# Kernel tuning notes

Hardware: AMD Instinct MI355X
Metric: run time of the kernel (lower is better)

The kernel has to match this reference:

```python
import jax, jax.numpy as jnp
import numpy as np

N = 50000
E = 625000
IN_NODE = 128
IN_EDGE = 64
H = 128
OUT = 112
L = 3


def setup_inputs() -> dict:
    key = jax.random.key(0)
    ks = jax.random.split(key, 16)
    s = lambda fan_in: 1.0 / np.sqrt(fan_in)
    inp = {
        "x": jax.random.normal(ks[0], (N, IN_NODE), jnp.float32),
        "edge_attr": jax.random.normal(ks[1], (E, IN_EDGE), jnp.float32),
        "edge_index": jax.random.randint(ks[2], (2, E), 0, N, jnp.int32),
        # encoders
        "node_W": jax.random.uniform(ks[3], (IN_NODE, H), jnp.float32, -s(IN_NODE), s(IN_NODE)),
        "node_b": jnp.zeros((H,), jnp.float32),
        "edge_W": jax.random.uniform(ks[4], (IN_EDGE, H), jnp.float32, -s(IN_EDGE), s(IN_EDGE)),
        "edge_b": jnp.zeros((H,), jnp.float32),
        # per-layer GINConv MLP params, stacked over layers
        "W1": jax.random.uniform(ks[5], (L, H, 2 * H), jnp.float32, -s(H), s(H)),
        "b1": jnp.zeros((L, 2 * H), jnp.float32),
        "W2": jax.random.uniform(ks[6], (L, 2 * H, H), jnp.float32, -s(2 * H), s(2 * H)),
        "b2": jnp.zeros((L, H), jnp.float32),
        "eps": jnp.zeros((L,), jnp.float32),
        # output head
        "lin_W": jax.random.uniform(ks[7], (H, OUT), jnp.float32, -s(H), s(H)),
        "lin_b": jnp.zeros((OUT,), jnp.float32),
    }
    return inp


def reference(x, edge_attr, edge_index, node_W, node_b, edge_W, edge_b,
              W1, b1, W2, b2, eps, lin_W, lin_b):
    src = edge_index[0]  # x_j gather indices (source nodes)
    dst = edge_index[1]  # scatter targets
    n = x.shape[0]

    x = x @ node_W + node_b                 # [N, H]
    ea = edge_attr @ edge_W + edge_b        # [E, H]

    # in-degree for mean aggregation (clamped at 1, zero-degree -> 0 agg)
    deg = jax.ops.segment_sum(jnp.ones((src.shape[0],), x.dtype), dst, num_segments=n)
    inv_deg = 1.0 / jnp.maximum(deg, 1.0)   # [N]

    for l in range(L):
        msg = x[src] + ea                                    # [E, H]
        agg = jax.ops.segment_sum(msg, dst, num_segments=n)  # [N, H]
        agg = agg * inv_deg[:, None]                         # mean
        h = (1.0 + eps[l]) * x + agg
        h = jax.nn.relu(h @ W1[l] + b1[l]) @ W2[l] + b2[l]   # GIN MLP
        x = jax.nn.relu(h)                                   # dropout is identity in eval

    return x @ lin_W + lin_b                 # [N, OUT]
```

## Files before the change

### kernel.cpp

```cpp
#include <hip/hip_runtime.h>


typedef unsigned short u16;
typedef unsigned int   u32;

using short8 = __attribute__((ext_vector_type(8))) short;
using f32x4  = __attribute__((ext_vector_type(4))) float;

__device__ __forceinline__ float b2f(u16 u) {
  union { u32 i; float f; } v; v.i = ((u32)u) << 16; return v.f;
}
__device__ __forceinline__ u16 f2b(float f) {
  union { float f; u32 i; } v; v.f = f;
  u32 i = v.i;
  return (u16)((i + 0x7FFFu + ((i >> 16) & 1u)) >> 16);
}

__global__ void sniff_kernel(const u16* __restrict__ xu, int* __restrict__ flag) {
  __shared__ int cnt;
  if (threadIdx.x == 0) cnt = 0;
  __syncthreads();
  int c = 0;
  for (int i = threadIdx.x; i < 1024; i += 256) {
    int e = (xu[i] >> 7) & 0xFF;
    if (e >= 100 && e <= 140) c++;
  }
  atomicAdd(&cnt, c);
  __syncthreads();
  if (threadIdx.x == 0) *flag = (cnt >= 820) ? 1 : 0;
}

__global__ void cvt_bf16_kernel(const void* __restrict__ src, u16* __restrict__ dst,
                                int n, const int* __restrict__ flag) {
  int i = blockIdx.x * 256 + threadIdx.x;
  if (i >= n) return;
  if (*flag) dst[i] = ((const u16*)src)[i];
  else       dst[i] = f2b(((const float*)src)[i]);
}

__global__ void cvt_f32_kernel(const void* __restrict__ src, float* __restrict__ dst,
                               int n, const int* __restrict__ flag) {
  int i = blockIdx.x * 256 + threadIdx.x;
  if (i >= n) return;
  if (*flag) dst[i] = b2f(((const u16*)src)[i]);
  else       dst[i] = ((const float*)src)[i];
}

__global__ void deg_kernel(const int* __restrict__ dst, int* __restrict__ deg, int e) {
  int i = blockIdx.x * 256 + threadIdx.x;
  if (i < e) atomicAdd(&deg[dst[i]], 1);
}

__global__ void scanA_kernel(const int* __restrict__ deg, int* __restrict__ rowptr,
                             float* __restrict__ invdeg, int* __restrict__ btot, int n) {
  __shared__ int wsum[4];
  int tid = threadIdx.x, lane = tid & 63, wid = tid >> 6;
  int i = blockIdx.x * 256 + tid;
  int v = (i < n) ? deg[i] : 0;
  int incl = v;
  #pragma unroll
  for (int off = 1; off < 64; off <<= 1) {
    int t = __shfl_up(incl, off, 64);
    if (lane >= off) incl += t;
  }
  if (lane == 63) wsum[wid] = incl;
  __syncthreads();
  int woff = 0;
  for (int w = 0; w < wid; ++w) woff += wsum[w];
  if (i < n) {
    rowptr[i] = woff + incl - v;
    invdeg[i] = 1.0f / fmaxf((float)v, 1.0f);
  }
  if (tid == 255) btot[blockIdx.x] = woff + incl;
}

__global__ void scanB_kernel(int* __restrict__ btot, int nb) {
  __shared__ int wsum[4];
  int tid = threadIdx.x, lane = tid & 63, wid = tid >> 6;
  int v = (tid < nb) ? btot[tid] : 0;
  int incl = v;
  #pragma unroll
  for (int off = 1; off < 64; off <<= 1) {
    int t = __shfl_up(incl, off, 64);
    if (lane >= off) incl += t;
  }
  if (lane == 63) wsum[wid] = incl;
  __syncthreads();
  int woff = 0;
  for (int w = 0; w < wid; ++w) woff += wsum[w];
  if (tid < nb) btot[tid] = woff + incl - v;
}

__global__ void scanC_kernel(int* __restrict__ rowptr, const int* __restrict__ btot,
                             int n, int e) {
  int i = blockIdx.x * 256 + threadIdx.x;
  if (i < n) rowptr[i] += btot[blockIdx.x];
  if (i == 0) rowptr[n] = e;
}

__global__ void fill_kernel(const int* __restrict__ src, const int* __restrict__ dst,
                            const int* __restrict__ rowptr, int* __restrict__ fillc,
                            int* __restrict__ csr_src, int* __restrict__ csr_eid, int e) {
  int i = blockIdx.x * 256 + threadIdx.x;
  if (i < e) {
    int d = dst[i];
    int p = rowptr[d] + atomicAdd(&fillc[d], 1);
    csr_src[p] = src[i];
    csr_eid[p] = i;
  }
}

template <int K, int N, int ACT, int FINAL>
__global__ __launch_bounds__(256) void gemm_kernel(const u16* __restrict__ A,
                                                   const u16* __restrict__ W,
                                                   const float* __restrict__ bias,
                                                   void* __restrict__ Cv, int M,
                                                   const int* __restrict__ flag) {
  constexpr int KC = 64;
  constexpr int KCP = KC + 8;
  constexpr int NF = N / 16;
  static_assert(K % KC == 0 && N % 16 == 0, "dims");
  __shared__ u16 WT[N * KCP];

  int tid = threadIdx.x, lane = tid & 63, wid = tid >> 6;
  int row0 = blockIdx.x * 64 + wid * 16;
  int arow = row0 + (lane & 15);
  if (arow >= M) arow = M - 1;

  f32x4 acc[NF];
  #pragma unroll
  for (int i = 0; i < NF; ++i) acc[i] = (f32x4){0.f, 0.f, 0.f, 0.f};

  for (int kc0 = 0; kc0 < K; kc0 += KC) {
    for (int idx = tid; idx < KC * N; idx += 256) {
      int kk = idx / N, nc = idx % N;
      WT[nc * KCP + kk] = W[(size_t)(kc0 + kk) * N + nc];
    }
    __syncthreads();
    const u16* Ab = A + (size_t)arow * K + kc0 + ((lane >> 4) * 8);
    #pragma unroll
    for (int ks = 0; ks < KC; ks += 32) {
      short8 a = *reinterpret_cast<const short8*>(Ab + ks);
      #pragma unroll
      for (int nf = 0; nf < NF; ++nf) {
        const u16* bp = &WT[(nf * 16 + (lane & 15)) * KCP + ks + ((lane >> 4) * 8)];
        short8 b = *reinterpret_cast<const short8*>(bp);
        acc[nf] = __builtin_amdgcn_mfma_f32_16x16x32_bf16(a, b, acc[nf], 0, 0, 0);
      }
    }
    __syncthreads();
  }

  int isbf = 1;
  if (FINAL) isbf = *flag;
  int crow0 = row0 + ((lane >> 4) * 4);
  #pragma unroll
  for (int nf = 0; nf < NF; ++nf) {
    int col = nf * 16 + (lane & 15);
    float bv = bias[col];
    #pragma unroll
    for (int r = 0; r < 4; ++r) {
      int crow = crow0 + r;
      if (crow < M) {
        float v = acc[nf][r] + bv;
        if (ACT) v = fmaxf(v, 0.f);
        size_t idx = (size_t)crow * N + col;
        if (FINAL && !isbf) ((float*)Cv)[idx] = v;
        else                ((u16*)Cv)[idx]   = f2b(v);
      }
    }
  }
}

__global__ __launch_bounds__(256) void sattr_sea_kernel(
    const void* __restrict__ ea, const int* __restrict__ rowptr,
    const int* __restrict__ csr_eid, const u16* __restrict__ edge_Wb,
    const float* __restrict__ edge_bf, const float* __restrict__ invdeg,
    float* __restrict__ seab, int nnodes, const int* __restrict__ flag) {
  __shared__ u16 w[64 * 128];
  int tid = threadIdx.x;
  for (int idx = tid; idx < 64 * 128; idx += 256) w[idx] = edge_Wb[idx];
  __syncthreads();
  int lane = tid & 63, wid = tid >> 6;
  int node = blockIdx.x * 4 + wid;
  if (node >= nnodes) return;
  int isbf = *flag;
  const u16*   eau = (const u16*)ea;
  const float* eaf = (const float*)ea;
  int r0 = rowptr[node], r1 = rowptr[node + 1];
  float acc = 0.f;
  for (int j = r0; j < r1; ++j) {
    size_t off = (size_t)csr_eid[j] * 64 + lane;
    acc += isbf ? b2f(eau[off]) : eaf[off];
  }
  float s0 = 0.f, s1 = 0.f;
  #pragma unroll 4
  for (int k = 0; k < 64; ++k) {
    float ak = __shfl(acc, k, 64);
    u32 wv = *reinterpret_cast<const u32*>(&w[k * 128 + lane * 2]);
    s0 += ak * b2f((u16)(wv & 0xffff));
    s1 += ak * b2f((u16)(wv >> 16));
  }
  float degf = (float)(r1 - r0);
  float iv = invdeg[node];
  seab[(size_t)node * 128 + lane * 2]     = (s0 + degf * edge_bf[lane * 2]) * iv;
  seab[(size_t)node * 128 + lane * 2 + 1] = (s1 + degf * edge_bf[lane * 2 + 1]) * iv;
}

__global__ __launch_bounds__(256) void agg_kernel(
    const u16* __restrict__ xcur, const int* __restrict__ rowptr,
    const int* __restrict__ csr_src, const float* __restrict__ invdeg,
    const float* __restrict__ seab, const float* __restrict__ epsf, int l,
    u16* __restrict__ h0, int nnodes) {
  int tid = threadIdx.x, lane = tid & 63, wid = tid >> 6;
  int node = blockIdx.x * 4 + wid;
  if (node >= nnodes) return;
  int r0 = rowptr[node], r1 = rowptr[node + 1];
  float a0 = 0.f, a1 = 0.f;
  for (int j = r0; j < r1; ++j) {
    int s = csr_src[j];
    u32 v = *reinterpret_cast<const u32*>(&xcur[(size_t)s * 128 + lane * 2]);
    a0 += b2f((u16)(v & 0xffff));
    a1 += b2f((u16)(v >> 16));
  }
  float epl = 1.0f + epsf[l];
  float iv = invdeg[node];
  u32 xv = *reinterpret_cast<const u32*>(&xcur[(size_t)node * 128 + lane * 2]);
  float h0v = epl * b2f((u16)(xv & 0xffff)) + a0 * iv + seab[(size_t)node * 128 + lane * 2];
  float h1v = epl * b2f((u16)(xv >> 16))    + a1 * iv + seab[(size_t)node * 128 + lane * 2 + 1];
  u32 packed = (u32)f2b(h0v) | ((u32)f2b(h1v) << 16);
  *reinterpret_cast<u32*>(&h0[(size_t)node * 128 + lane * 2]) = packed;
}

extern "C" void kernel_launch(void* const* d_in, const int* in_sizes, int n_in,
                              void* d_out, int out_size, void* d_ws, size_t ws_size,
                              hipStream_t stream) {
  const void* x_in  = d_in[0];
  const void* eattr = d_in[1];
  const int*  eidx  = (const int*)d_in[2];
  const void* nodeW = d_in[3];
  const void* nodeb = d_in[4];
  const void* edgeW = d_in[5];
  const void* edgeb = d_in[6];
  const void* W1    = d_in[7];
  const void* b1    = d_in[8];
  const void* W2    = d_in[9];
  const void* b2    = d_in[10];
  const void* eps   = d_in[11];
  const void* linW  = d_in[12];
  const void* linb  = d_in[13];

  int nn = in_sizes[0] / 128;
  int ne = in_sizes[2] / 2;

  char* ws = (char*)d_ws;
  size_t off = 0;
  auto alloc = [&](size_t b) { size_t r = off; off += (b + 255) & ~(size_t)255; return r; };
  int*    flag    = (int*)(ws + alloc(4));
  int*    deg     = (int*)(ws + alloc((size_t)nn * 4));
  int*    fillc   = (int*)(ws + alloc((size_t)nn * 4));
  int*    rowptr  = (int*)(ws + alloc((size_t)(nn + 1) * 4));
  float*  invdeg  = (float*)(ws + alloc((size_t)nn * 4));
  int*    btot    = (int*)(ws + alloc(256 * 4));
  int*    csr_src = (int*)(ws + alloc((size_t)ne * 4));
  int*    csr_eid = (int*)(ws + alloc((size_t)ne * 4));
  float*  seab    = (float*)(ws + alloc((size_t)nn * 128 * 4));
  u16*    xb      = (u16*)(ws + alloc((size_t)nn * 128 * 2));
  u16*    xcur    = (u16*)(ws + alloc((size_t)nn * 128 * 2));
  u16*    h0      = (u16*)(ws + alloc((size_t)nn * 128 * 2));
  u16*    tbuf    = (u16*)(ws + alloc((size_t)nn * 256 * 2));
  u16*    nodeWb  = (u16*)(ws + alloc(128 * 128 * 2));
  u16*    edgeWb  = (u16*)(ws + alloc(64 * 128 * 2));
  u16*    W1b     = (u16*)(ws + alloc((size_t)3 * 128 * 256 * 2));
  u16*    W2b     = (u16*)(ws + alloc((size_t)3 * 256 * 128 * 2));
  u16*    linWb   = (u16*)(ws + alloc(128 * 112 * 2));
  float*  nodebf  = (float*)(ws + alloc(128 * 4));
  float*  edgebf  = (float*)(ws + alloc(128 * 4));
  float*  b1f     = (float*)(ws + alloc(3 * 256 * 4));
  float*  b2f_    = (float*)(ws + alloc(3 * 128 * 4));
  float*  epsf    = (float*)(ws + alloc(3 * 4));
  float*  linbf   = (float*)(ws + alloc(112 * 4));

  hipMemsetAsync(deg, 0, (size_t)nn * 4, stream);
  hipMemsetAsync(fillc, 0, (size_t)nn * 4, stream);

  sniff_kernel<<<1, 256, 0, stream>>>((const u16*)x_in, flag);

  auto cvtb = [&](const void* s, u16* d, int n) {
    cvt_bf16_kernel<<<(n + 255) / 256, 256, 0, stream>>>(s, d, n, flag);
  };
  auto cvtf = [&](const void* s, float* d, int n) {
    cvt_f32_kernel<<<(n + 255) / 256, 256, 0, stream>>>(s, d, n, flag);
  };
  cvtb(x_in, xb, nn * 128);
  cvtb(nodeW, nodeWb, 128 * 128);
  cvtb(edgeW, edgeWb, 64 * 128);
  cvtb(W1, W1b, 3 * 128 * 256);
  cvtb(W2, W2b, 3 * 256 * 128);
  cvtb(linW, linWb, 128 * 112);
  cvtf(nodeb, nodebf, 128);
  cvtf(edgeb, edgebf, 128);
  cvtf(b1, b1f, 3 * 256);
  cvtf(b2, b2f_, 3 * 128);
  cvtf(eps, epsf, 3);
  cvtf(linb, linbf, 112);

  int eb = (ne + 255) / 256;
  int nb = (nn + 255) / 256;
  deg_kernel<<<eb, 256, 0, stream>>>(eidx + ne, deg, ne);
  scanA_kernel<<<nb, 256, 0, stream>>>(deg, rowptr, invdeg, btot, nn);
  scanB_kernel<<<1, 256, 0, stream>>>(btot, nb);
  scanC_kernel<<<nb, 256, 0, stream>>>(rowptr, btot, nn, ne);
  fill_kernel<<<eb, 256, 0, stream>>>(eidx, eidx + ne, rowptr, fillc, csr_src, csr_eid, ne);

  int gb = (nn + 63) / 64;
  gemm_kernel<128, 128, 0, 0><<<gb, 256, 0, stream>>>(xb, nodeWb, nodebf, xcur, nn, flag);
  sattr_sea_kernel<<<(nn + 3) / 4, 256, 0, stream>>>(eattr, rowptr, csr_eid, edgeWb, edgebf,
                                                     invdeg, seab, nn, flag);
  for (int l = 0; l < 3; ++l) {
    agg_kernel<<<(nn + 3) / 4, 256, 0, stream>>>(xcur, rowptr, csr_src, invdeg, seab, epsf, l, h0, nn);
    gemm_kernel<128, 256, 1, 0><<<gb, 256, 0, stream>>>(h0, W1b + (size_t)l * 128 * 256,
                                                        b1f + l * 256, tbuf, nn, flag);
    gemm_kernel<256, 128, 1, 0><<<gb, 256, 0, stream>>>(tbuf, W2b + (size_t)l * 256 * 128,
                                                        b2f_ + l * 128, xcur, nn, flag);
  }
  gemm_kernel<128, 112, 0, 1><<<gb, 256, 0, stream>>>(xcur, linWb, linbf, d_out, nn, flag);
}
```

Before: 867.7 us.

## Pre-transpose weights, scatter edge attrs atomically, unroll aggregation gather

Weights are converted and transposed once up front, so the GEMM loads its shared-memory tile with 16-byte vectors instead of scalar transposing loads. The per-node CSR gather of edge attributes plus the per-node shuffle matvec is replaced by an atomic scatter of edge_attr into a per-node fp32 sum, followed by an MFMA GEMM (MODE 2) that applies inv-degree and the degree-gated bias. The csr_eid array is dropped. The aggregation gather is unrolled by four with independent accumulators to raise memory-level parallelism, and the bias conversions are batched into one launch. The atomic float scatter adds nondeterministic summation order and contention on high-degree nodes.

Result: faster. 743.7 us (-14.3%).

```diff
diff --git a/kernel.cpp b/kernel.cpp
--- a/kernel.cpp
+++ b/kernel.cpp
@@ -38,12 +38,24 @@
   else       dst[i] = f2b(((const float*)src)[i]);
 }
 
-__global__ void cvt_f32_kernel(const void* __restrict__ src, float* __restrict__ dst,
-                               int n, const int* __restrict__ flag) {
-  int i = blockIdx.x * 256 + threadIdx.x;
-  if (i >= n) return;
-  if (*flag) dst[i] = b2f(((const u16*)src)[i]);
-  else       dst[i] = ((const float*)src)[i];
+__global__ void transpose_cvt_kernel(const void* __restrict__ src, u16* __restrict__ dst,
+                                     int K, int N, int total, const int* __restrict__ flag) {
+  int i = blockIdx.x * 256 + threadIdx.x;
+  if (i >= total) return;
+  int kn = K * N;
+  int l = i / kn, r = i - l * kn;
+  int k = r / N, n = r - k * N;
+  u16 v = (*flag) ? ((const u16*)src)[i] : f2b(((const float*)src)[i]);
+  dst[(size_t)l * kn + n * K + k] = v;
+}
+
+struct BiasJobs { const void* src[6]; float* dst[6]; int len[6]; };
+__global__ void cvt_bias_kernel(BiasJobs j, const int* __restrict__ flag) {
+  int b = blockIdx.x;
+  int isbf = *flag;
+  for (int i = threadIdx.x; i < j.len[b]; i += 256) {
+    j.dst[b][i] = isbf ? b2f(((const u16*)j.src[b])[i]) : ((const float*)j.src[b])[i];
+  }
 }
 
 __global__ void deg_kernel(const int* __restrict__ dst, int* __restrict__ deg, int e) {
@@ -100,27 +112,40 @@
 
 __global__ void fill_kernel(const int* __restrict__ src, const int* __restrict__ dst,
                             const int* __restrict__ rowptr, int* __restrict__ fillc,
-                            int* __restrict__ csr_src, int* __restrict__ csr_eid, int e) {
+                            int* __restrict__ csr_src, int e) {
   int i = blockIdx.x * 256 + threadIdx.x;
   if (i < e) {
     int d = dst[i];
     int p = rowptr[d] + atomicAdd(&fillc[d], 1);
     csr_src[p] = src[i];
-    csr_eid[p] = i;
-  }
-}
-
-template <int K, int N, int ACT, int FINAL>
-__global__ __launch_bounds__(256) void gemm_kernel(const u16* __restrict__ A,
-                                                   const u16* __restrict__ W,
-                                                   const float* __restrict__ bias,
-                                                   void* __restrict__ Cv, int M,
-                                                   const int* __restrict__ flag) {
+  }
+}
+
+__global__ __launch_bounds__(256) void scatter_kernel(
+    const void* __restrict__ ea, const int* __restrict__ dst,
+    float* __restrict__ sattr, int e, const int* __restrict__ flag) {
+  int eg = blockIdx.x * 4 + (threadIdx.x >> 6);
+  int lane = threadIdx.x & 63;
+  if (eg >= e) return;
+  int d = dst[eg];
+  float v;
+  if (*flag) v = b2f(((const u16*)ea)[(size_t)eg * 64 + lane]);
+  else       v = ((const float*)ea)[(size_t)eg * 64 + lane];
+  atomicAdd(&sattr[(size_t)d * 64 + lane], v);
+}
+
+template <int K, int N, int ACT, int MODE>
+__global__ __launch_bounds__(256) void gemm_kernel(
+    const void* __restrict__ Av, const u16* __restrict__ WT,
+    const float* __restrict__ bias, void* __restrict__ Cv, int M,
+    const int* __restrict__ flag, const float* __restrict__ rowscale,
+    const int* __restrict__ degp) {
   constexpr int KC = 64;
   constexpr int KCP = KC + 8;
   constexpr int NF = N / 16;
+  constexpr int NV = N * KC / 8;
   static_assert(K % KC == 0 && N % 16 == 0, "dims");
-  __shared__ u16 WT[N * KCP];
+  __shared__ u16 WS[N * KCP];
 
   int tid = threadIdx.x, lane = tid & 63, wid = tid >> 6;
   int row0 = blockIdx.x * 64 + wid * 16;
@@ -132,18 +157,29 @@
   for (int i = 0; i < NF; ++i) acc[i] = (f32x4){0.f, 0.f, 0.f, 0.f};
 
   for (int kc0 = 0; kc0 < K; kc0 += KC) {
-    for (int idx = tid; idx < KC * N; idx += 256) {
-      int kk = idx / N, nc = idx % N;
-      WT[nc * KCP + kk] = W[(size_t)(kc0 + kk) * N + nc];
+    #pragma unroll
+    for (int v = tid; v < NV; v += 256) {
+      int n = v >> 3, k8 = (v & 7) << 3;
+      *reinterpret_cast<short8*>(&WS[n * KCP + k8]) =
+          *reinterpret_cast<const short8*>(&WT[(size_t)n * K + kc0 + k8]);
     }
     __syncthreads();
-    const u16* Ab = A + (size_t)arow * K + kc0 + ((lane >> 4) * 8);
     #pragma unroll
     for (int ks = 0; ks < KC; ks += 32) {
-      short8 a = *reinterpret_cast<const short8*>(Ab + ks);
+      short8 a;
+      if (MODE == 2) {
+        const float* Af = (const float*)Av + (size_t)arow * K + kc0 + ((lane >> 4) * 8) + ks;
+        f32x4 a0 = *reinterpret_cast<const f32x4*>(Af);
+        f32x4 a1 = *reinterpret_cast<const f32x4*>(Af + 4);
+        #pragma unroll
+        for (int q = 0; q < 4; ++q) { a[q] = (short)f2b(a0[q]); a[q + 4] = (short)f2b(a1[q]); }
+      } else {
+        const u16* Ab = (const u16*)Av + (size_t)arow * K + kc0 + ((lane >> 4) * 8) + ks;
+        a = *reinterpret_cast<const short8*>(Ab);
+      }
       #pragma unroll
       for (int nf = 0; nf < NF; ++nf) {
-        const u16* bp = &WT[(nf * 16 + (lane & 15)) * KCP + ks + ((lane >> 4) * 8)];
+        const u16* bp = &WS[(nf * 16 + (lane & 15)) * KCP + ks + ((lane >> 4) * 8)];
         short8 b = *reinterpret_cast<const short8*>(bp);
         acc[nf] = __builtin_amdgcn_mfma_f32_16x16x32_bf16(a, b, acc[nf], 0, 0, 0);
       }
@@ -152,7 +188,7 @@
   }
 
   int isbf = 1;
-  if (FINAL) isbf = *flag;
+  if (MODE == 1) isbf = *flag;
   int crow0 = row0 + ((lane >> 4) * 4);
   #pragma unroll
   for (int nf = 0; nf < NF; ++nf) {
@@ -162,49 +198,19 @@
     for (int r = 0; r < 4; ++r) {
       int crow = crow0 + r;
       if (crow < M) {
-        float v = acc[nf][r] + bv;
-        if (ACT) v = fmaxf(v, 0.f);
         size_t idx = (size_t)crow * N + col;
-        if (FINAL && !isbf) ((float*)Cv)[idx] = v;
-        else                ((u16*)Cv)[idx]   = f2b(v);
+        if (MODE == 2) {
+          float v = acc[nf][r] * rowscale[crow] + (degp[crow] > 0 ? bv : 0.f);
+          ((float*)Cv)[idx] = v;
+        } else {
+          float v = acc[nf][r] + bv;
+          if (ACT) v = fmaxf(v, 0.f);
+          if (MODE == 1 && !isbf) ((float*)Cv)[idx] = v;
+          else                    ((u16*)Cv)[idx]   = f2b(v);
+        }
       }
     }
   }
-}
-
-__global__ __launch_bounds__(256) void sattr_sea_kernel(
-    const void* __restrict__ ea, const int* __restrict__ rowptr,
-    const int* __restrict__ csr_eid, const u16* __restrict__ edge_Wb,
-    const float* __restrict__ edge_bf, const float* __restrict__ invdeg,
-    float* __restrict__ seab, int nnodes, const int* __restrict__ flag) {
-  __shared__ u16 w[64 * 128];
-  int tid = threadIdx.x;
-  for (int idx = tid; idx < 64 * 128; idx += 256) w[idx] = edge_Wb[idx];
-  __syncthreads();
-  int lane = tid & 63, wid = tid >> 6;
-  int node = blockIdx.x * 4 + wid;
-  if (node >= nnodes) return;
-  int isbf = *flag;
-  const u16*   eau = (const u16*)ea;
-  const float* eaf = (const float*)ea;
-  int r0 = rowptr[node], r1 = rowptr[node + 1];
-  float acc = 0.f;
-  for (int j = r0; j < r1; ++j) {
-    size_t off = (size_t)csr_eid[j] * 64 + lane;
-    acc += isbf ? b2f(eau[off]) : eaf[off];
-  }
-  float s0 = 0.f, s1 = 0.f;
-  #pragma unroll 4
-  for (int k = 0; k < 64; ++k) {
-    float ak = __shfl(acc, k, 64);
-    u32 wv = *reinterpret_cast<const u32*>(&w[k * 128 + lane * 2]);
-    s0 += ak * b2f((u16)(wv & 0xffff));
-    s1 += ak * b2f((u16)(wv >> 16));
-  }
-  float degf = (float)(r1 - r0);
-  float iv = invdeg[node];
-  seab[(size_t)node * 128 + lane * 2]     = (s0 + degf * edge_bf[lane * 2]) * iv;
-  seab[(size_t)node * 128 + lane * 2 + 1] = (s1 + degf * edge_bf[lane * 2 + 1]) * iv;
 }
 
 __global__ __launch_bounds__(256) void agg_kernel(
@@ -215,17 +221,31 @@
   int tid = threadIdx.x, lane = tid & 63, wid = tid >> 6;
   int node = blockIdx.x * 4 + wid;
   if (node >= nnodes) return;
+  const u32* xc = (const u32*)xcur;
   int r0 = rowptr[node], r1 = rowptr[node + 1];
-  float a0 = 0.f, a1 = 0.f;
-  for (int j = r0; j < r1; ++j) {
+  float p0 = 0.f, p1 = 0.f, q0 = 0.f, q1 = 0.f, s0 = 0.f, s1 = 0.f, t0 = 0.f, t1 = 0.f;
+  int j = r0;
+  for (; j + 4 <= r1; j += 4) {
+    int sa = csr_src[j], sb = csr_src[j + 1], sc = csr_src[j + 2], sd = csr_src[j + 3];
+    u32 va = xc[(size_t)sa * 64 + lane];
+    u32 vb = xc[(size_t)sb * 64 + lane];
+    u32 vc = xc[(size_t)sc * 64 + lane];
+    u32 vd = xc[(size_t)sd * 64 + lane];
+    p0 += b2f((u16)(va & 0xffff)); p1 += b2f((u16)(va >> 16));
+    q0 += b2f((u16)(vb & 0xffff)); q1 += b2f((u16)(vb >> 16));
+    s0 += b2f((u16)(vc & 0xffff)); s1 += b2f((u16)(vc >> 16));
+    t0 += b2f((u16)(vd & 0xffff)); t1 += b2f((u16)(vd >> 16));
+  }
+  for (; j < r1; ++j) {
     int s = csr_src[j];
-    u32 v = *reinterpret_cast<const u32*>(&xcur[(size_t)s * 128 + lane * 2]);
-    a0 += b2f((u16)(v & 0xffff));
-    a1 += b2f((u16)(v >> 16));
-  }
+    u32 v = xc[(size_t)s * 64 + lane];
+    p0 += b2f((u16)(v & 0xffff)); p1 += b2f((u16)(v >> 16));
+  }
+  float a0 = (p0 + q0) + (s0 + t0);
+  float a1 = (p1 + q1) + (s1 + t1);
   float epl = 1.0f + epsf[l];
   float iv = invdeg[node];
-  u32 xv = *reinterpret_cast<const u32*>(&xcur[(size_t)node * 128 + lane * 2]);
+  u32 xv = xc[(size_t)node * 64 + lane];
   float h0v = epl * b2f((u16)(xv & 0xffff)) + a0 * iv + seab[(size_t)node * 128 + lane * 2];
   float h1v = epl * b2f((u16)(xv >> 16))    + a1 * iv + seab[(size_t)node * 128 + lane * 2 + 1];
   u32 packed = (u32)f2b(h0v) | ((u32)f2b(h1v) << 16);
@@ -263,17 +283,17 @@
   float*  invdeg  = (float*)(ws + alloc((size_t)nn * 4));
   int*    btot    = (int*)(ws + alloc(256 * 4));
   int*    csr_src = (int*)(ws + alloc((size_t)ne * 4));
-  int*    csr_eid = (int*)(ws + alloc((size_t)ne * 4));
+  float*  sattr   = (float*)(ws + alloc((size_t)nn * 64 * 4));
   float*  seab    = (float*)(ws + alloc((size_t)nn * 128 * 4));
   u16*    xb      = (u16*)(ws + alloc((size_t)nn * 128 * 2));
   u16*    xcur    = (u16*)(ws + alloc((size_t)nn * 128 * 2));
   u16*    h0      = (u16*)(ws + alloc((size_t)nn * 128 * 2));
   u16*    tbuf    = (u16*)(ws + alloc((size_t)nn * 256 * 2));
-  u16*    nodeWb  = (u16*)(ws + alloc(128 * 128 * 2));
-  u16*    edgeWb  = (u16*)(ws + alloc(64 * 128 * 2));
-  u16*    W1b     = (u16*)(ws + alloc((size_t)3 * 128 * 256 * 2));
-  u16*    W2b     = (u16*)(ws + alloc((size_t)3 * 256 * 128 * 2));
-  u16*    linWb   = (u16*)(ws + alloc(128 * 112 * 2));
+  u16*    nodeWT  = (u16*)(ws + alloc(128 * 128 * 2));
+  u16*    edgeWT  = (u16*)(ws + alloc(64 * 128 * 2));
+  u16*    W1T     = (u16*)(ws + alloc((size_t)3 * 128 * 256 * 2));
+  u16*    W2T     = (u16*)(ws + alloc((size_t)3 * 256 * 128 * 2));
+  u16*    linWT   = (u16*)(ws + alloc(128 * 112 * 2));
   float*  nodebf  = (float*)(ws + alloc(128 * 4));
   float*  edgebf  = (float*)(ws + alloc(128 * 4));
   float*  b1f     = (float*)(ws + alloc(3 * 256 * 4));
@@ -283,27 +303,29 @@
 
   hipMemsetAsync(deg, 0, (size_t)nn * 4, stream);
   hipMemsetAsync(fillc, 0, (size_t)nn * 4, stream);
+  hipMemsetAsync(sattr, 0, (size_t)nn * 64 * 4, stream);
 
   sniff_kernel<<<1, 256, 0, stream>>>((const u16*)x_in, flag);
 
-  auto cvtb = [&](const void* s, u16* d, int n) {
-    cvt_bf16_kernel<<<(n + 255) / 256, 256, 0, stream>>>(s, d, n, flag);
+  cvt_bf16_kernel<<<(nn * 128 + 255) / 256, 256, 0, stream>>>(x_in, xb, nn * 128, flag);
+  auto tcv = [&](const void* s, u16* d, int K, int N, int L) {
+    int tot = L * K * N;
+    transpose_cvt_kernel<<<(tot + 255) / 256, 256, 0, stream>>>(s, d, K, N, tot, flag);
   };
-  auto cvtf = [&](const void* s, float* d, int n) {
-    cvt_f32_kernel<<<(n + 255) / 256, 256, 0, stream>>>(s, d, n, flag);
-  };
-  cvtb(x_in, xb, nn * 128);
-  cvtb(nodeW, nodeWb, 128 * 128);
-  cvtb(edgeW, edgeWb, 64 * 128);
-  cvtb(W1, W1b, 3 * 128 * 256);
-  cvtb(W2, W2b, 3 * 256 * 128);
-  cvtb(linW, linWb, 128 * 112);
-  cvtf(nodeb, nodebf, 128);
-  cvtf(edgeb, edgebf, 128);
-  cvtf(b1, b1f, 3 * 256);
-  cvtf(b2, b2f_, 3 * 128);
-  cvtf(eps, epsf, 3);
-  cvtf(linb, linbf, 112);
+  tcv(nodeW, nodeWT, 128, 128, 1);
+  tcv(edgeW, edgeWT, 64, 128, 1);
+  tcv(W1, W1T, 128, 256, 3);
+  tcv(W2, W2T, 256, 128, 3);
+  tcv(linW, linWT, 128, 112, 1);
+
+  BiasJobs bj;
+  bj.src[0] = nodeb; bj.dst[0] = nodebf; bj.len[0] = 128;
+  bj.src[1] = edgeb; bj.dst[1] = edgebf; bj.len[1] = 128;
+  bj.src[2] = b1;    bj.dst[2] = b1f;    bj.len[2] = 3 * 256;
+  bj.src[3] = b2;    bj.dst[3] = b2f_;   bj.len[3] = 3 * 128;
+  bj.src[4] = eps;   bj.dst[4] = epsf;   bj.len[4] = 3;
+  bj.src[5] = linb;  bj.dst[5] = linbf;  bj.len[5] = 112;
+  cvt_bias_kernel<<<6, 256, 0, stream>>>(bj, flag);
 
   int eb = (ne + 255) / 256;
   int nb = (nn + 255) / 256;
@@ -311,18 +333,20 @@
   scanA_kernel<<<nb, 256, 0, stream>>>(deg, rowptr, invdeg, btot, nn);
   scanB_kernel<<<1, 256, 0, stream>>>(btot, nb);
   scanC_kernel<<<nb, 256, 0, stream>>>(rowptr, btot, nn, ne);
-  fill_kernel<<<eb, 256, 0, stream>>>(eidx, eidx + ne, rowptr, fillc, csr_src, csr_eid, ne);
+  fill_kernel<<<eb, 256, 0, stream>>>(eidx, eidx + ne, rowptr, fillc, csr_src, ne);
+
+  scatter_kernel<<<(ne + 3) / 4, 256, 0, stream>>>(eattr, eidx + ne, sattr, ne, flag);
 
   int gb = (nn + 63) / 64;
-  gemm_kernel<128, 128, 0, 0><<<gb, 256, 0, stream>>>(xb, nodeWb, nodebf, xcur, nn, flag);
-  sattr_sea_kernel<<<(nn + 3) / 4, 256, 0, stream>>>(eattr, rowptr, csr_eid, edgeWb, edgebf,
-                                                     invdeg, seab, nn, flag);
+  gemm_kernel<128, 128, 0, 0><<<gb, 256, 0, stream>>>(xb, nodeWT, nodebf, xcur, nn, flag, nullptr, nullptr);
+  gemm_kernel<64, 128, 0, 2><<<gb, 256, 0, stream>>>(sattr, edgeWT, edgebf, seab, nn, flag, invdeg, deg);
+
   for (int l = 0; l < 3; ++l) {
     agg_kernel<<<(nn + 3) / 4, 256, 0, stream>>>(xcur, rowptr, csr_src, invdeg, seab, epsf, l, h0, nn);
-    gemm_kernel<128, 256, 1, 0><<<gb, 256, 0, stream>>>(h0, W1b + (size_t)l * 128 * 256,
-                                                        b1f + l * 256, tbuf, nn, flag);
-    gemm_kernel<256, 128, 1, 0><<<gb, 256, 0, stream>>>(tbuf, W2b + (size_t)l * 256 * 128,
-                                                        b2f_ + l * 128, xcur, nn, flag);
-  }
-  gemm_kernel<128, 112, 0, 1><<<gb, 256, 0, stream>>>(xcur, linWb, linbf, d_out, nn, flag);
-}
+    gemm_kernel<128, 256, 1, 0><<<gb, 256, 0, stream>>>(h0, W1T + (size_t)l * 128 * 256,
+                                                        b1f + l * 256, tbuf, nn, flag, nullptr, nullptr);
+    gemm_kernel<256, 128, 1, 0><<<gb, 256, 0, stream>>>(tbuf, W2T + (size_t)l * 256 * 128,
+                                                        b2f_ + l * 128, xcur, nn, flag, nullptr, nullptr);
+  }
+  gemm_kernel<128, 112, 0, 1><<<gb, 256, 0, stream>>>(xcur, linWT, linbf, d_out, nn, flag, nullptr, nullptr);
+}
```
